# Kernel optimization log

Hardware: AMD Instinct MI355X
Metric: run time of the kernel (lower is better)

## Reference

```python
import jax, jax.numpy as jnp
import numpy as np

N = 50000        # num nodes
E = 800000       # num edges (avg degree 16)
IN_DIM = 64
OUT_DIM = 64
PE_DIM = 24
HEADS = 2
HID = OUT_DIM * HEADS  # 128


def setup_inputs() -> dict:
    key = jax.random.key(0)
    ks = jax.random.split(key, 16)
    std = 0.1  # trunc_normal_(std=0.1) init in the torch module
    return {
        "x": jax.random.normal(ks[0], (N, IN_DIM), jnp.float32),
        "pe_index": jax.random.randint(ks[1], (2, E), 0, N, jnp.int32),
        "pe_val": jax.random.normal(ks[2], (E, PE_DIM), jnp.float32),
        # edge-weight MLP (blocks): input proj, one residual FFN block, final proj
        "W_in": jax.random.normal(ks[3], (PE_DIM, HID), jnp.float32) * std,
        "b_in": jnp.zeros((HID,), jnp.float32),
        "W1": jax.random.normal(ks[4], (HID, HID), jnp.float32) * std,
        "b1": jnp.zeros((HID,), jnp.float32),
        "W2": jax.random.normal(ks[5], (HID, HID), jnp.float32) * std,
        "b2": jnp.zeros((HID,), jnp.float32),
        "W_fin": jax.random.normal(ks[6], (HID, HID), jnp.float32) * std,
        "b_fin": jnp.zeros((HID,), jnp.float32),
        # node feature -> multi-head projection
        "W_x": jax.random.normal(ks[7], (IN_DIM, HID), jnp.float32) * std,
        "b_x": jnp.zeros((HID,), jnp.float32),
        # per-head output bias
        "head_bias": jnp.zeros((1, HEADS, OUT_DIM), jnp.float32),
        # final out projection
        "W_out": jax.random.normal(ks[8], (HID, OUT_DIM), jnp.float32) * std,
        "b_out": jnp.zeros((OUT_DIM,), jnp.float32),
    }


def _edge_mlp(pe, W_in, b_in, W1, b1, W2, b2, W_fin, b_fin):
    # Linear(pe_dim->hid), then residual block [GELU, Linear, GELU, Linear, +res], then Linear(hid->hid)
    g = lambda t: jax.nn.gelu(t, approximate=False)  # torch nn.GELU default = exact erf
    x0 = pe @ W_in + b_in                     # [E, HID]
    h = g(x0) @ W1 + b1
    h = g(h) @ W2 + b2
    x0 = h + x0                               # ResidualLayer: x + x_res
    return x0 @ W_fin + b_fin                 # [E, HID]


def reference(x, pe_index, pe_val, W_in, b_in, W1, b1, W2, b2, W_fin, b_fin,
              W_x, b_x, head_bias, W_out, b_out):
    tgt = pe_index[0]  # messages aggregate to edge_index[0]
    src = pe_index[1]
    score = _edge_mlp(pe_val, W_in, b_in, W1, b1, W2, b2, W_fin, b_fin)
    score = score.reshape(-1, HEADS, OUT_DIM)                 # [E, H, D]
    xh = (x @ W_x + b_x).reshape(-1, HEADS, OUT_DIM)          # [N, H, D]
    msg = xh[src] * score                                     # gather-multiply
    wV = jax.ops.segment_sum(msg, tgt, num_segments=N)        # scatter-add [N, H, D]
    deg = jax.ops.segment_sum(jnp.ones((msg.shape[0],), jnp.float32), tgt, num_segments=N)
    wV = wV / jnp.maximum(deg, 1.0)[:, None, None]            # average=True -> mean aggregation
    h = (wV + head_bias).reshape(-1, HEADS * OUT_DIM)
    return h @ W_out + b_out                                  # out_proj: [N, OUT_DIM]
```

## Files before the change

kernel.cpp:

```cpp
#include <hip/hip_runtime.h>
#include <hip/hip_bf16.h>
#include <math.h>

#define NN 50000
#define EE 800000
#define HID 128
#define PED 24
#define IND 64
#define OUTD 64
#define EBLK 128
#define AKS 136

typedef short bf16x8 __attribute__((ext_vector_type(8)));
typedef float f32x4 __attribute__((ext_vector_type(4)));

__device__ __forceinline__ float gelu_fast(float x) {
    float x2 = x * x;
    float t = __builtin_fmaf(x2, -0.07135481627f, -1.5957691216f);
    float e = __expf(x * t);
    return x * __builtin_amdgcn_rcpf(1.0f + e);
}
__device__ __forceinline__ unsigned short f2bf(float f) {
    unsigned int u = __float_as_uint(f);
    u = (u + 0x7fffu + ((u >> 16) & 1u)) >> 16;
    return (unsigned short)u;
}
__device__ __forceinline__ unsigned int pkbf2(float a, float b) {
    __hip_bfloat162 h = __float22bfloat162_rn(make_float2(a, b));
    return *reinterpret_cast<unsigned int*>(&h);
}
__device__ __forceinline__ float bflo(unsigned int u) {
    return __uint_as_float(u << 16);
}
__device__ __forceinline__ float bfhi(unsigned int u) {
    return __uint_as_float(u & 0xffff0000u);
}

__global__ __launch_bounds__(256) void pre_kernel(
    const float* __restrict__ x, const float* __restrict__ W_x,
    const float* __restrict__ b_x, unsigned short* __restrict__ xhb,
    const float* __restrict__ W_in, const float* __restrict__ W1,
    const float* __restrict__ W2, const float* __restrict__ Wf,
    unsigned short* __restrict__ WT_in, unsigned short* __restrict__ WT1,
    unsigned short* __restrict__ WT2, unsigned short* __restrict__ WTf,
    float* __restrict__ wV, int* __restrict__ cnt) {
    int bx = blockIdx.x;
    if (bx < 6250) {
        int gid = bx * 256 + threadIdx.x;
        int n = gid >> 5;
        int q = gid & 31;
        *(float4*)&wV[(size_t)n * HID + q * 4] = make_float4(0.f, 0.f, 0.f, 0.f);
        const float* xr = x + (size_t)n * IND;
        float4 acc = *(const float4*)&b_x[q * 4];
#pragma unroll 8
        for (int k = 0; k < IND; k++) {
            float xk = xr[k];
            float4 w = *(const float4*)&W_x[k * HID + q * 4];
            acc.x += xk * w.x; acc.y += xk * w.y;
            acc.z += xk * w.z; acc.w += xk * w.w;
        }
        uint2 p;
        p.x = pkbf2(acc.x, acc.y);
        p.y = pkbf2(acc.z, acc.w);
        ((uint2*)&xhb[(size_t)n * HID])[q] = p;
    } else {
        int idx = (bx - 6250) * 256 + threadIdx.x;
        if (idx < NN) cnt[idx] = 0;
        if (idx < 4096) {
            int j = idx >> 5, k = idx & 31;
            WT_in[idx] = f2bf(k < PED ? W_in[k * HID + j] : 0.f);
        } else if (idx < 4096 + 16384) {
            int i = idx - 4096; int j = i >> 7, k = i & 127;
            WT1[i] = f2bf(W1[k * HID + j]);
        } else if (idx < 4096 + 32768) {
            int i = idx - 4096 - 16384; int j = i >> 7, k = i & 127;
            WT2[i] = f2bf(W2[k * HID + j]);
        } else if (idx < 4096 + 49152) {
            int i = idx - 4096 - 32768; int j = i >> 7, k = i & 127;
            WTf[i] = f2bf(Wf[k * HID + j]);
        }
    }
}

__global__ __launch_bounds__(256) void hist_kernel(const int* __restrict__ pe_idx,
                                                   int* __restrict__ cnt) {
    int e = blockIdx.x * 256 + threadIdx.x;
    if (e < EE) atomicAdd(&cnt[pe_idx[e]], 1);
}

__global__ __launch_bounds__(1024) void scan_kernel(const int* __restrict__ cnt,
                                                    int* __restrict__ woff) {
    __shared__ int s_w[16];
    int tid = threadIdx.x;
    const int chunk = (NN + 1023) / 1024;
    int base = tid * chunk;
    int end = base + chunk; if (end > NN) end = NN;
    int s = 0;
    for (int i = base; i < end; i++) s += cnt[i];
    int v = s;
    int lane = tid & 63, wid = tid >> 6;
#pragma unroll
    for (int d = 1; d < 64; d <<= 1) {
        int u = __shfl_up(v, d, 64);
        if (lane >= d) v += u;
    }
    if (lane == 63) s_w[wid] = v;
    __syncthreads();
    if (tid < 16) {
        int wv = s_w[tid];
#pragma unroll
        for (int d = 1; d < 16; d <<= 1) {
            int u = __shfl_up(wv, d, 64);
            if (tid >= d) wv += u;
        }
        s_w[tid] = wv;
    }
    __syncthreads();
    int exc = v - s + (wid ? s_w[wid - 1] : 0);
    int run = exc;
    for (int i = base; i < end; i++) { woff[i] = run; run += cnt[i]; }
}

__global__ __launch_bounds__(256) void scatter_kernel(const int* __restrict__ pe_idx,
                                                      int* __restrict__ woff,
                                                      int* __restrict__ perm) {
    int e = blockIdx.x * 256 + threadIdx.x;
    if (e < EE) {
        int t = pe_idx[e];
        int p = atomicAdd(&woff[t], 1);
        perm[p] = e;
    }
}

__global__ __launch_bounds__(512, 4) void edge_kernel(
    const float* __restrict__ pe_val, const int* __restrict__ pe_idx,
    const int* __restrict__ perm, const unsigned short* __restrict__ xhb,
    const unsigned short* __restrict__ WT_in, const unsigned short* __restrict__ WT1,
    const unsigned short* __restrict__ WT2, const unsigned short* __restrict__ WTf,
    const float* __restrict__ b_in, const float* __restrict__ b1,
    const float* __restrict__ b2, const float* __restrict__ bfin,
    float* __restrict__ wV) {
    __shared__ __align__(16) unsigned short s_act[EBLK][AKS];
    __shared__ __align__(16) unsigned short s_W[HID][AKS];
    __shared__ int s_eid[EBLK], s_tgt[EBLK], s_src[EBLK];
    float* s_msg = (float*)&s_W[0][0];

    const int tid = threadIdx.x;
    const int lane = tid & 63;
    const int w = tid >> 6;
    const int cg = w & 3;
    const int eh = w >> 2;
    const int ebase = eh * 64;
    const int l15 = lane & 15;
    const int quad = lane >> 4;
    const long b0 = (long)blockIdx.x * EBLK;

    if (tid < EBLK) {
        int eid = perm[b0 + tid];
        s_eid[tid] = eid;
        s_tgt[tid] = pe_idx[eid];
        s_src[tid] = pe_idx[EE + eid];
    }
#pragma unroll
    for (int i = 0; i < 4; i++) {
        int idx = tid + i * 512; int r = idx >> 4, seg = idx & 15;
        *(uint4*)&s_W[r][seg * 8] = *(const uint4*)&WT1[r * HID + seg * 8];
    }
    __syncthreads();
#pragma unroll
    for (int i = 0; i < 4; i++) {
        int idx = tid + i * 512; int e = idx >> 4, k2 = idx & 15;
        float2 v = make_float2(0.f, 0.f);
        if (k2 < 12) v = *(const float2*)&pe_val[(size_t)s_eid[e] * PED + k2 * 2];
        *(unsigned int*)&s_act[e][k2 * 2] = pkbf2(v.x, v.y);
    }
    __syncthreads();

    f32x4 C[2][4];
    f32x4 x0s[2][4];

    {
        float4 ba = *(const float4*)&b_in[(2 * cg + 0) * 16 + quad * 4];
        float4 bb = *(const float4*)&b_in[(2 * cg + 1) * 16 + quad * 4];
        f32x4 ci0 = {ba.x, ba.y, ba.z, ba.w};
        f32x4 ci1 = {bb.x, bb.y, bb.z, bb.w};
        bf16x8 a0 = *(const bf16x8*)&WT_in[((2 * cg + 0) * 16 + l15) * 32 + quad * 8];
        bf16x8 a1 = *(const bf16x8*)&WT_in[((2 * cg + 1) * 16 + l15) * 32 + quad * 8];
#pragma unroll
        for (int u = 0; u < 4; u++) {
            bf16x8 bfr = *(const bf16x8*)&s_act[ebase + u * 16 + l15][quad * 8];
            C[0][u] = __builtin_amdgcn_mfma_f32_16x16x32_bf16(a0, bfr, ci0, 0, 0, 0);
            C[1][u] = __builtin_amdgcn_mfma_f32_16x16x32_bf16(a1, bfr, ci1, 0, 0, 0);
        }
    }
    __syncthreads();
#pragma unroll
    for (int t = 0; t < 2; t++) {
        int ch0 = (2 * cg + t) * 16 + quad * 4;
#pragma unroll
        for (int u = 0; u < 4; u++) {
            int e = ebase + u * 16 + l15;
            f32x4 c = C[t][u];
            x0s[t][u] = c;
            uint2 p;
            p.x = pkbf2(gelu_fast(c[0]), gelu_fast(c[1]));
            p.y = pkbf2(gelu_fast(c[2]), gelu_fast(c[3]));
            *(uint2*)&s_act[e][ch0] = p;
        }
    }
    __syncthreads();

#define GEMM128(BIAS)                                                          \
    {                                                                          \
        float4 ba_ = *(const float4*)&(BIAS)[(2 * cg + 0) * 16 + quad * 4];    \
        float4 bb_ = *(const float4*)&(BIAS)[(2 * cg + 1) * 16 + quad * 4];    \
        f32x4 ci0 = {ba_.x, ba_.y, ba_.z, ba_.w};                              \
        f32x4 ci1 = {bb_.x, bb_.y, bb_.z, bb_.w};                              \
        _Pragma("unroll") for (int u = 0; u < 4; u++) {                        \
            C[0][u] = ci0; C[1][u] = ci1;                                      \
        }                                                                      \
        _Pragma("unroll") for (int ks = 0; ks < 4; ks++) {                     \
            bf16x8 a0 = *(const bf16x8*)&s_W[(2 * cg + 0) * 16 + l15]          \
                                            [ks * 32 + quad * 8];              \
            bf16x8 a1 = *(const bf16x8*)&s_W[(2 * cg + 1) * 16 + l15]          \
                                            [ks * 32 + quad * 8];              \
            _Pragma("unroll") for (int u = 0; u < 4; u++) {                    \
                bf16x8 bfr = *(const bf16x8*)&s_act[ebase + u * 16 + l15]      \
                                                   [ks * 32 + quad * 8];       \
                C[0][u] = __builtin_amdgcn_mfma_f32_16x16x32_bf16(a0, bfr,     \
                                                                  C[0][u], 0, 0, 0); \
                C[1][u] = __builtin_amdgcn_mfma_f32_16x16x32_bf16(a1, bfr,     \
                                                                  C[1][u], 0, 0, 0); \
            }                                                                  \
        }                                                                      \
    }

#define STAGE_W(WT)                                                            \
    _Pragma("unroll") for (int i = 0; i < 4; i++) {                            \
        int idx = tid + i * 512; int r = idx >> 4, seg = idx & 15;             \
        *(uint4*)&s_W[r][seg * 8] = *(const uint4*)&(WT)[r * HID + seg * 8];   \
    }

    GEMM128(b1);
    __syncthreads();
#pragma unroll
    for (int t = 0; t < 2; t++) {
        int ch0 = (2 * cg + t) * 16 + quad * 4;
#pragma unroll
        for (int u = 0; u < 4; u++) {
            int e = ebase + u * 16 + l15;
            f32x4 c = C[t][u];
            uint2 p;
            p.x = pkbf2(gelu_fast(c[0]), gelu_fast(c[1]));
            p.y = pkbf2(gelu_fast(c[2]), gelu_fast(c[3]));
            *(uint2*)&s_act[e][ch0] = p;
        }
    }
    STAGE_W(WT2);
    __syncthreads();

    GEMM128(b2);
    __syncthreads();
#pragma unroll
    for (int t = 0; t < 2; t++) {
        int ch0 = (2 * cg + t) * 16 + quad * 4;
#pragma unroll
        for (int u = 0; u < 4; u++) {
            int e = ebase + u * 16 + l15;
            f32x4 c = C[t][u];
            f32x4 x0 = x0s[t][u];
            uint2 p;
            p.x = pkbf2(c[0] + x0[0], c[1] + x0[1]);
            p.y = pkbf2(c[2] + x0[2], c[3] + x0[3]);
            *(uint2*)&s_act[e][ch0] = p;
        }
    }
    STAGE_W(WTf);
    __syncthreads();

    GEMM128(bfin);
    uint2 xva[4];
#pragma unroll
    for (int i = 0; i < 4; i++) {
        int idx = tid + i * 512; int e = idx >> 5, c4 = idx & 31;
        xva[i] = ((const uint2*)&xhb[(size_t)s_src[e] * HID])[c4];
    }
    __syncthreads();
#pragma unroll
    for (int t = 0; t < 2; t++) {
        int ch0 = (2 * cg + t) * 16 + quad * 4;
#pragma unroll
        for (int u = 0; u < 4; u++) {
            int e = ebase + u * 16 + l15;
            f32x4 c = C[t][u];
            uint2 p;
            p.x = pkbf2(c[0], c[1]);
            p.y = pkbf2(c[2], c[3]);
            *(uint2*)&s_act[e][ch0] = p;
        }
    }
    __syncthreads();

#pragma unroll
    for (int i = 0; i < 4; i++) {
        int idx = tid + i * 512;
        int e = idx >> 5, c4 = idx & 31;
        uint2 xv = xva[i];
        uint2 sv = *(const uint2*)&s_act[e][c4 * 4];
        float4 m;
        m.x = bflo(xv.x) * bflo(sv.x);
        m.y = bfhi(xv.x) * bfhi(sv.x);
        m.z = bflo(xv.y) * bflo(sv.y);
        m.w = bfhi(xv.y) * bfhi(sv.y);
        *(float4*)&s_msg[e * HID + c4 * 4] = m;
    }
    uint2 xvb[4];
#pragma unroll
    for (int i = 0; i < 4; i++) {
        int idx = tid + (4 + i) * 512; int e = idx >> 5, c4 = idx & 31;
        xvb[i] = ((const uint2*)&xhb[(size_t)s_src[e] * HID])[c4];
    }
    __syncthreads();

    if (tid < 256) {
        const int h = tid >> 7;
        const int c = tid & 127;
        const int e0 = h * 32;
        float acc = 0.f;
        int prev = s_tgt[e0];
        bool firstseg = true;
        for (int e = e0; e < e0 + 32; e++) {
            int tg = s_tgt[e];
            if (tg != prev) {
                if (firstseg) atomicAdd(&wV[(size_t)prev * HID + c], acc);
                else          wV[(size_t)prev * HID + c] = acc;
                firstseg = false;
                acc = 0.f;
                prev = tg;
            }
            acc += s_msg[e * HID + c];
        }
        atomicAdd(&wV[(size_t)prev * HID + c], acc);
    }
    __syncthreads();

#pragma unroll
    for (int i = 0; i < 4; i++) {
        int idx = tid + (4 + i) * 512;
        int e = idx >> 5, c4 = idx & 31;
        uint2 xv = xvb[i];
        uint2 sv = *(const uint2*)&s_act[e][c4 * 4];
        float4 m;
        m.x = bflo(xv.x) * bflo(sv.x);
        m.y = bfhi(xv.x) * bfhi(sv.x);
        m.z = bflo(xv.y) * bflo(sv.y);
        m.w = bfhi(xv.y) * bfhi(sv.y);
        *(float4*)&s_msg[(e - 64) * HID + c4 * 4] = m;
    }
    __syncthreads();

    if (tid < 256) {
        const int h = tid >> 7;
        const int c = tid & 127;
        const int e0 = 64 + h * 32;
        float acc = 0.f;
        int prev = s_tgt[e0];
        bool firstseg = true;
        for (int e = e0; e < e0 + 32; e++) {
            int tg = s_tgt[e];
            if (tg != prev) {
                if (firstseg) atomicAdd(&wV[(size_t)prev * HID + c], acc);
                else          wV[(size_t)prev * HID + c] = acc;
                firstseg = false;
                acc = 0.f;
                prev = tg;
            }
            acc += s_msg[(e - 64) * HID + c];
        }
        atomicAdd(&wV[(size_t)prev * HID + c], acc);
    }
#undef GEMM128
#undef STAGE_W
}

__global__ __launch_bounds__(256) void out_kernel(
    const float* __restrict__ wV, const int* __restrict__ cnt,
    const float* __restrict__ head_bias, const float* __restrict__ W_out,
    const float* __restrict__ b_out, float* __restrict__ out) {
    int gid = blockIdx.x * 256 + threadIdx.x;
    int n = gid >> 4;
    int q = gid & 15;
    if (n >= NN) return;
    float inv = 1.0f / fmaxf((float)cnt[n], 1.0f);
    const float* wr = wV + (size_t)n * HID;
    float4 acc = *(const float4*)&b_out[q * 4];
#pragma unroll 4
    for (int k = 0; k < HID; k++) {
        float hv = wr[k] * inv + head_bias[k];
        float4 wv4 = *(const float4*)&W_out[k * OUTD + q * 4];
        acc.x += hv * wv4.x; acc.y += hv * wv4.y;
        acc.z += hv * wv4.z; acc.w += hv * wv4.w;
    }
    *(float4*)&out[(size_t)n * OUTD + q * 4] = acc;
}

extern "C" void kernel_launch(void* const* d_in, const int* in_sizes, int n_in,
                              void* d_out, int out_size, void* d_ws, size_t ws_size,
                              hipStream_t stream) {
    const float* x      = (const float*)d_in[0];
    const int*   pe_idx = (const int*)d_in[1];
    const float* pe_val = (const float*)d_in[2];
    const float* W_in   = (const float*)d_in[3];
    const float* b_in   = (const float*)d_in[4];
    const float* W1     = (const float*)d_in[5];
    const float* b1     = (const float*)d_in[6];
    const float* W2     = (const float*)d_in[7];
    const float* b2     = (const float*)d_in[8];
    const float* Wf     = (const float*)d_in[9];
    const float* bfin   = (const float*)d_in[10];
    const float* W_x    = (const float*)d_in[11];
    const float* b_x    = (const float*)d_in[12];
    const float* hb     = (const float*)d_in[13];
    const float* W_out  = (const float*)d_in[14];
    const float* b_out  = (const float*)d_in[15];
    float* out = (float*)d_out;

    float* wV   = (float*)d_ws;
    int*   cnt  = (int*)(wV + (size_t)NN * HID);
    int*   woff = cnt + NN;
    int*   perm = woff + NN;
    unsigned short* WT_in = (unsigned short*)(perm + EE);
    unsigned short* WT1   = WT_in + 128 * 32;
    unsigned short* WT2   = WT1 + 128 * 128;
    unsigned short* WTf   = WT2 + 128 * 128;
    unsigned short* xhb   = WTf + 128 * 128;

    pre_kernel<<<6250 + 208, 256, 0, stream>>>(x, W_x, b_x, xhb,
                                               W_in, W1, W2, Wf,
                                               WT_in, WT1, WT2, WTf, wV, cnt);
    hist_kernel<<<(EE + 255) / 256, 256, 0, stream>>>(pe_idx, cnt);
    scan_kernel<<<1, 1024, 0, stream>>>(cnt, woff);
    scatter_kernel<<<(EE + 255) / 256, 256, 0, stream>>>(pe_idx, woff, perm);

    edge_kernel<<<EE / EBLK, 512, 0, stream>>>(pe_val, pe_idx, perm, xhb,
                                               WT_in, WT1, WT2, WTf,
                                               b_in, b1, b2, bfin, wV);

    out_kernel<<<(NN * 16 + 255) / 256, 256, 0, stream>>>(wV, cnt, hb, W_out,
                                                          b_out, out);
}
```

Baseline: 632.5 us.

## Vectorize CSR build kernels, prefetch next weights, pack residual to bf16, add setprio

The histogram and scatter kernels now process four edges per thread through int4 loads, and the scan reads its chunk with vector loads. In the edge kernel, the next layer's weight tile is loaded into registers before the current GEMM, so global latency overlaps the MFMA work. The residual x0 is held as packed bf16 instead of fp32 to cut register pressure, and a barrier is removed by reading perm directly. s_setprio is placed around the MFMA loops; bf16 rounding of the residual adds some precision loss.

```diff
diff --git a/kernel.cpp b/kernel.cpp
--- a/kernel.cpp
+++ b/kernel.cpp
@@ -84,19 +84,33 @@
 
 __global__ __launch_bounds__(256) void hist_kernel(const int* __restrict__ pe_idx,
                                                    int* __restrict__ cnt) {
-    int e = blockIdx.x * 256 + threadIdx.x;
-    if (e < EE) atomicAdd(&cnt[pe_idx[e]], 1);
+    int e4 = blockIdx.x * 256 + threadIdx.x;
+    if (e4 < EE / 4) {
+        int4 t = *(const int4*)&pe_idx[e4 * 4];
+        atomicAdd(&cnt[t.x], 1);
+        atomicAdd(&cnt[t.y], 1);
+        atomicAdd(&cnt[t.z], 1);
+        atomicAdd(&cnt[t.w], 1);
+    }
 }
 
 __global__ __launch_bounds__(1024) void scan_kernel(const int* __restrict__ cnt,
                                                     int* __restrict__ woff) {
     __shared__ int s_w[16];
     int tid = threadIdx.x;
-    const int chunk = (NN + 1023) / 1024;
+    const int chunk = 52;
     int base = tid * chunk;
     int end = base + chunk; if (end > NN) end = NN;
     int s = 0;
-    for (int i = base; i < end; i++) s += cnt[i];
+    if (base + chunk <= NN) {
+#pragma unroll
+        for (int i = 0; i < 13; i++) {
+            int4 v4 = *(const int4*)&cnt[base + i * 4];
+            s += v4.x + v4.y + v4.z + v4.w;
+        }
+    } else {
+        for (int i = base; i < end; i++) s += cnt[i];
+    }
     int v = s;
     int lane = tid & 63, wid = tid >> 6;
 #pragma unroll
@@ -124,11 +138,14 @@
 __global__ __launch_bounds__(256) void scatter_kernel(const int* __restrict__ pe_idx,
                                                       int* __restrict__ woff,
                                                       int* __restrict__ perm) {
-    int e = blockIdx.x * 256 + threadIdx.x;
-    if (e < EE) {
-        int t = pe_idx[e];
-        int p = atomicAdd(&woff[t], 1);
-        perm[p] = e;
+    int e4 = blockIdx.x * 256 + threadIdx.x;
+    if (e4 < EE / 4) {
+        int4 t = *(const int4*)&pe_idx[e4 * 4];
+        int e = e4 * 4;
+        perm[atomicAdd(&woff[t.x], 1)] = e + 0;
+        perm[atomicAdd(&woff[t.y], 1)] = e + 1;
+        perm[atomicAdd(&woff[t.z], 1)] = e + 2;
+        perm[atomicAdd(&woff[t.w], 1)] = e + 3;
     }
 }
 
@@ -142,7 +159,7 @@
     float* __restrict__ wV) {
     __shared__ __align__(16) unsigned short s_act[EBLK][AKS];
     __shared__ __align__(16) unsigned short s_W[HID][AKS];
-    __shared__ int s_eid[EBLK], s_tgt[EBLK], s_src[EBLK];
+    __shared__ int s_tgt[EBLK], s_src[EBLK];
     float* s_msg = (float*)&s_W[0][0];
 
     const int tid = threadIdx.x;
@@ -157,7 +174,6 @@
 
     if (tid < EBLK) {
         int eid = perm[b0 + tid];
-        s_eid[tid] = eid;
         s_tgt[tid] = pe_idx[eid];
         s_src[tid] = pe_idx[EE + eid];
     }
@@ -166,18 +182,20 @@
         int idx = tid + i * 512; int r = idx >> 4, seg = idx & 15;
         *(uint4*)&s_W[r][seg * 8] = *(const uint4*)&WT1[r * HID + seg * 8];
     }
-    __syncthreads();
 #pragma unroll
     for (int i = 0; i < 4; i++) {
         int idx = tid + i * 512; int e = idx >> 4, k2 = idx & 15;
         float2 v = make_float2(0.f, 0.f);
-        if (k2 < 12) v = *(const float2*)&pe_val[(size_t)s_eid[e] * PED + k2 * 2];
+        if (k2 < 12) {
+            int eid = perm[b0 + e];
+            v = *(const float2*)&pe_val[(size_t)eid * PED + k2 * 2];
+        }
         *(unsigned int*)&s_act[e][k2 * 2] = pkbf2(v.x, v.y);
     }
     __syncthreads();
 
     f32x4 C[2][4];
-    f32x4 x0s[2][4];
+    uint2 x0pk[2][4];
 
     {
         float4 ba = *(const float4*)&b_in[(2 * cg + 0) * 16 + quad * 4];
@@ -186,12 +204,14 @@
         f32x4 ci1 = {bb.x, bb.y, bb.z, bb.w};
         bf16x8 a0 = *(const bf16x8*)&WT_in[((2 * cg + 0) * 16 + l15) * 32 + quad * 8];
         bf16x8 a1 = *(const bf16x8*)&WT_in[((2 * cg + 1) * 16 + l15) * 32 + quad * 8];
+        __builtin_amdgcn_s_setprio(1);
 #pragma unroll
         for (int u = 0; u < 4; u++) {
             bf16x8 bfr = *(const bf16x8*)&s_act[ebase + u * 16 + l15][quad * 8];
             C[0][u] = __builtin_amdgcn_mfma_f32_16x16x32_bf16(a0, bfr, ci0, 0, 0, 0);
             C[1][u] = __builtin_amdgcn_mfma_f32_16x16x32_bf16(a1, bfr, ci1, 0, 0, 0);
         }
+        __builtin_amdgcn_s_setprio(0);
     }
     __syncthreads();
 #pragma unroll
@@ -201,7 +221,8 @@
         for (int u = 0; u < 4; u++) {
             int e = ebase + u * 16 + l15;
             f32x4 c = C[t][u];
-            x0s[t][u] = c;
+            x0pk[t][u].x = pkbf2(c[0], c[1]);
+            x0pk[t][u].y = pkbf2(c[2], c[3]);
             uint2 p;
             p.x = pkbf2(gelu_fast(c[0]), gelu_fast(c[1]));
             p.y = pkbf2(gelu_fast(c[2]), gelu_fast(c[3]));
@@ -219,6 +240,7 @@
         _Pragma("unroll") for (int u = 0; u < 4; u++) {                        \
             C[0][u] = ci0; C[1][u] = ci1;                                      \
         }                                                                      \
+        __builtin_amdgcn_s_setprio(1);                                         \
         _Pragma("unroll") for (int ks = 0; ks < 4; ks++) {                     \
             bf16x8 a0 = *(const bf16x8*)&s_W[(2 * cg + 0) * 16 + l15]          \
                                             [ks * 32 + quad * 8];              \
@@ -233,14 +255,22 @@
                                                                   C[1][u], 0, 0, 0); \
             }                                                                  \
         }                                                                      \
-    }
-
-#define STAGE_W(WT)                                                            \
+        __builtin_amdgcn_s_setprio(0);                                         \
+    }
+
+#define PREFETCH_W(WT, DST)                                                    \
+    _Pragma("unroll") for (int i = 0; i < 4; i++) {                            \
+        int idx = tid + i * 512;                                               \
+        DST[i] = *(const uint4*)&(WT)[(idx >> 4) * HID + (idx & 15) * 8];      \
+    }
+#define WRITE_W(SRC)                                                           \
     _Pragma("unroll") for (int i = 0; i < 4; i++) {                            \
         int idx = tid + i * 512; int r = idx >> 4, seg = idx & 15;             \
-        *(uint4*)&s_W[r][seg * 8] = *(const uint4*)&(WT)[r * HID + seg * 8];   \
-    }
-
+        *(uint4*)&s_W[r][seg * 8] = SRC[i];                                    \
+    }
+
+    uint4 wpre[4];
+    PREFETCH_W(WT2, wpre);
     GEMM128(b1);
     __syncthreads();
 #pragma unroll
@@ -256,9 +286,10 @@
             *(uint2*)&s_act[e][ch0] = p;
         }
     }
-    STAGE_W(WT2);
-    __syncthreads();
-
+    WRITE_W(wpre);
+    __syncthreads();
+
+    PREFETCH_W(WTf, wpre);
     GEMM128(b2);
     __syncthreads();
 #pragma unroll
@@ -268,14 +299,13 @@
         for (int u = 0; u < 4; u++) {
             int e = ebase + u * 16 + l15;
             f32x4 c = C[t][u];
-            f32x4 x0 = x0s[t][u];
             uint2 p;
-            p.x = pkbf2(c[0] + x0[0], c[1] + x0[1]);
-            p.y = pkbf2(c[2] + x0[2], c[3] + x0[3]);
+            p.x = pkbf2(c[0] + bflo(x0pk[t][u].x), c[1] + bfhi(x0pk[t][u].x));
+            p.y = pkbf2(c[2] + bflo(x0pk[t][u].y), c[3] + bfhi(x0pk[t][u].y));
             *(uint2*)&s_act[e][ch0] = p;
         }
     }
-    STAGE_W(WTf);
+    WRITE_W(wpre);
     __syncthreads();
 
     GEMM128(bfin);
@@ -380,7 +410,8 @@
         atomicAdd(&wV[(size_t)prev * HID + c], acc);
     }
 #undef GEMM128
-#undef STAGE_W
+#undef PREFETCH_W
+#undef WRITE_W
 }
 
 __global__ __launch_bounds__(256) void out_kernel(
@@ -438,9 +469,9 @@
     pre_kernel<<<6250 + 208, 256, 0, stream>>>(x, W_x, b_x, xhb,
                                                W_in, W1, W2, Wf,
                                                WT_in, WT1, WT2, WTf, wV, cnt);
-    hist_kernel<<<(EE + 255) / 256, 256, 0, stream>>>(pe_idx, cnt);
+    hist_kernel<<<(EE / 4 + 255) / 256, 256, 0, stream>>>(pe_idx, cnt);
     scan_kernel<<<1, 1024, 0, stream>>>(cnt, woff);
-    scatter_kernel<<<(EE + 255) / 256, 256, 0, stream>>>(pe_idx, woff, perm);
+    scatter_kernel<<<(EE / 4 + 255) / 256, 256, 0, stream>>>(pe_idx, woff, perm);
 
     edge_kernel<<<EE / EBLK, 512, 0, stream>>>(pe_val, pe_idx, perm, xhb,
                                                WT_in, WT1, WT2, WTf,
```

Measured after the change: 693.5 us. 1.1x slower.
